# Performance work log

Hardware: AMD Instinct MI355X
Metric: run time of the kernel (lower is better)

The kernel has to match this reference:

```python
import jax, jax.numpy as jnp
import numpy as np

B, T, D, HD = 256, 256, 512, 64  # batch, seq_len(SEQ_LEN), EMBED_DIM, head_dim


def setup_inputs() -> dict:
    key = jax.random.key(0)
    k1, k2, k3, k4 = jax.random.split(key, 4)
    scale = D ** -0.5  # roughly matches nn.Linear init variance
    return {
        "x": jax.random.normal(k1, (B, T, D), dtype=jnp.float32),
        "Wq": jax.random.normal(k2, (HD, D), dtype=jnp.float32) * scale,
        "Wk": jax.random.normal(k3, (HD, D), dtype=jnp.float32) * scale,
        "Wv": jax.random.normal(k4, (HD, D), dtype=jnp.float32) * scale,
    }


def reference(x, Wq, Wk, Wv):
    # q,k,v: [B, T, HD]  (torch Linear: x @ W.T, no bias)
    q = jnp.einsum("btd,hd->bth", x, Wq)
    k = jnp.einsum("btd,hd->bth", x, Wk)
    v = jnp.einsum("btd,hd->bth", x, Wv)
    head_dim = Wq.shape[0]
    # scores: [B, T, T], scaled by head_dim^-0.5
    scores = jnp.einsum("bqh,bkh->bqk", q, k) * (head_dim ** -0.5)
    T_ = x.shape[1]
    causal = jnp.tril(jnp.ones((T_, T_), dtype=bool))  # tril[:T,:T] == 0 -> -inf
    scores = jnp.where(causal, scores, -jnp.inf)
    attn = jax.nn.softmax(scores, axis=-1)
    # dropout is identity in eval mode (reference baseline)
    return jnp.einsum("bqk,bkh->bqh", attn, v)
```

## Files before the change

kernel.cpp:

```cpp
#include <hip/hip_runtime.h>
#include <hip/hip_bf16.h>
#include <stdint.h>

#define NB 256
#define NT 256
#define ND 512
#define NH 64

typedef __bf16 bf16;
typedef __bf16 bf16x4 __attribute__((ext_vector_type(4)));
typedef __bf16 bf16x8 __attribute__((ext_vector_type(8)));
typedef float f32x4 __attribute__((ext_vector_type(4)));

static __device__ __forceinline__ f32x4 mfma16(bf16x8 a, bf16x8 b, f32x4 c) {
    return __builtin_amdgcn_mfma_f32_16x16x32_bf16(a, b, c, 0, 0, 0);
}

static __device__ __forceinline__ bf16x8 cvt8(f32x4 a, f32x4 b) {
    bf16x8 r;
    r[0] = (bf16)a.x; r[1] = (bf16)a.y; r[2] = (bf16)a.z; r[3] = (bf16)a.w;
    r[4] = (bf16)b.x; r[5] = (bf16)b.y; r[6] = (bf16)b.z; r[7] = (bf16)b.w;
    return r;
}

__global__ __launch_bounds__(256) void wconv_kernel(
        const float* __restrict__ Wq, const float* __restrict__ Wk,
        const float* __restrict__ Wv, bf16* __restrict__ wbf) {
    int idx = (blockIdx.x * 256 + threadIdx.x) * 4;
    const float* src;
    if (idx < 64 * ND)       src = Wq + idx;
    else if (idx < 128 * ND) src = Wk + (idx - 64 * ND);
    else                     src = Wv + (idx - 128 * ND);
    f32x4 v = *reinterpret_cast<const f32x4*>(src);
    bf16x4 o;
    o[0] = (bf16)v.x; o[1] = (bf16)v.y; o[2] = (bf16)v.z; o[3] = (bf16)v.w;
    *reinterpret_cast<bf16x4*>(wbf + idx) = o;
}

__global__ __launch_bounds__(256) void qkv_gemm_kernel(
        const float* __restrict__ x, const bf16* __restrict__ wbf,
        bf16* __restrict__ qws, bf16* __restrict__ kws, bf16* __restrict__ vt) {
    __shared__ alignas(16) char lds[65536];
    const int t = threadIdx.x;
    const int lane = t & 63, wave = t >> 6;
    const long m0 = (long)blockIdx.x * 64;

    {
        const int srow = t >> 2, skc = (t & 3) * 16;
        const int ssw = (srow & 7) << 4;
        const float* xsrc = x + (m0 + srow) * ND + skc;
        #pragma unroll
        for (int kk = 0; kk < ND; kk += 64) {
            f32x4 a = *reinterpret_cast<const f32x4*>(xsrc + kk);
            f32x4 b = *reinterpret_cast<const f32x4*>(xsrc + kk + 4);
            f32x4 c = *reinterpret_cast<const f32x4*>(xsrc + kk + 8);
            f32x4 d = *reinterpret_cast<const f32x4*>(xsrc + kk + 12);
            int base = srow * 1024 + (kk + skc) * 2;
            *reinterpret_cast<bf16x8*>(lds + (base ^ ssw)) = cvt8(a, b);
            *reinterpret_cast<bf16x8*>(lds + ((base + 16) ^ ssw)) = cvt8(c, d);
        }
    }
    __syncthreads();

    f32x4 acc[4][3] = {};
    const int l15 = lane & 15, g8 = (lane >> 4) * 8;

    #pragma unroll 4
    for (int chunk = 0; chunk < 16; ++chunk) {
        const int kg = chunk * 32 + g8;
        bf16x8 Af[4];
        #pragma unroll
        for (int ri = 0; ri < 4; ++ri) {
            int row = ri * 16 + l15;
            Af[ri] = *reinterpret_cast<const bf16x8*>(
                lds + ((row * 1024 + kg * 2) ^ ((row & 7) << 4)));
        }
        #pragma unroll
        for (int ci = 0; ci < 3; ++ci) {
            int n = wave * 48 + ci * 16 + l15;
            bf16x8 Bf = *reinterpret_cast<const bf16x8*>(wbf + n * ND + kg);
            #pragma unroll
            for (int ri = 0; ri < 4; ++ri)
                acc[ri][ci] = mfma16(Af[ri], Bf, acc[ri][ci]);
        }
    }

    const int b = blockIdx.x >> 2;
    const int tb = (blockIdx.x & 3) * 64;
    #pragma unroll
    for (int ci = 0; ci < 3; ++ci) {
        int n = wave * 48 + ci * 16 + l15;
        int sel = n >> 6, hd = n & 63;
        #pragma unroll
        for (int ri = 0; ri < 4; ++ri) {
            #pragma unroll
            for (int r = 0; r < 4; ++r) {
                int trow = tb + ri * 16 + (lane >> 4) * 4 + r;
                long grow = m0 + ri * 16 + (lane >> 4) * 4 + r;
                float val = acc[ri][ci][r];
                if (sel == 0)      qws[grow * NH + hd] = (bf16)(val * 0.125f);
                else if (sel == 1) kws[grow * NH + hd] = (bf16)val;
                else               vt[((long)b * NH + hd) * NT + trow] = (bf16)val;
            }
        }
    }
}

__global__ __launch_bounds__(64) void attn_kernel(
        const bf16* __restrict__ qws, const bf16* __restrict__ kws,
        const bf16* __restrict__ vt, float* __restrict__ out) {
    __shared__ alignas(16) char plds[8192];
    const int lane = threadIdx.x & 63;
    const int l15 = lane & 15, g = lane >> 4;
    const int qt = blockIdx.x, b = blockIdx.y;
    const long bbase = (long)b * NT;

    const int nct = qt + 1;
    const int nch = (nct + 1) >> 1;

    bf16x8 Qf[2];
    {
        long qrow = bbase + qt * 16 + l15;
        const bf16* qsrc = qws + qrow * NH + g * 8;
        Qf[0] = *reinterpret_cast<const bf16x8*>(qsrc);
        Qf[1] = *reinterpret_cast<const bf16x8*>(qsrc + 32);
    }

    const int qrow0 = qt * 16 + g * 4;
    float sum[4] = {0.f, 0.f, 0.f, 0.f};
    f32x4 O[4] = {};

    #pragma unroll
    for (int ch = 0; ch < 8; ++ch) {
        if (ch < nch) {
            const int t0 = 2 * ch, t1 = 2 * ch + 1;
            const bool t1v = (t1 < nct);
            f32x4 S0 = {}, S1 = {};
            {
                const bf16* kb0 = kws + (bbase + t0 * 16 + l15) * NH + g * 8;
                S0 = mfma16(Qf[0], *reinterpret_cast<const bf16x8*>(kb0), S0);
                S0 = mfma16(Qf[1], *reinterpret_cast<const bf16x8*>(kb0 + 32), S0);
                if (t1v) {
                    const bf16* kb1 = kb0 + 16 * NH;
                    S1 = mfma16(Qf[0], *reinterpret_cast<const bf16x8*>(kb1), S1);
                    S1 = mfma16(Qf[1], *reinterpret_cast<const bf16x8*>(kb1 + 32), S1);
                }
            }
            const int c0 = t0 * 16 + l15, c1 = c0 + 16;
            #pragma unroll
            for (int r = 0; r < 4; ++r) {
                int rowp = g * 4 + r;
                int sw = (rowp & 7) << 4;
                float p0 = (c0 <= qrow0 + r) ? __expf(S0[r]) : 0.0f;
                sum[r] += p0;
                *reinterpret_cast<bf16*>(plds + ((rowp * 512 + c0 * 2) ^ sw)) = (bf16)p0;
                float p1 = (t1v && c1 <= qrow0 + r) ? __expf(S1[r]) : 0.0f;
                sum[r] += p1;
                *reinterpret_cast<bf16*>(plds + ((rowp * 512 + c1 * 2) ^ sw)) = (bf16)p1;
            }
            const int k0 = ch * 32 + g * 8;
            bf16x8 Pf = *reinterpret_cast<const bf16x8*>(
                plds + ((l15 * 512 + k0 * 2) ^ ((l15 & 7) << 4)));
            #pragma unroll
            for (int cb = 0; cb < 4; ++cb) {
                int hd = cb * 16 + l15;
                bf16x8 Vf = *reinterpret_cast<const bf16x8*>(
                    vt + ((long)b * NH + hd) * NT + k0);
                O[cb] = mfma16(Pf, Vf, O[cb]);
            }
        }
    }

    #pragma unroll
    for (int r = 0; r < 4; ++r) {
        sum[r] += __shfl_xor(sum[r], 1);
        sum[r] += __shfl_xor(sum[r], 2);
        sum[r] += __shfl_xor(sum[r], 4);
        sum[r] += __shfl_xor(sum[r], 8);
        sum[r] = 1.0f / sum[r];
    }

    #pragma unroll
    for (int cb = 0; cb < 4; ++cb) {
        int hd = cb * 16 + l15;
        #pragma unroll
        for (int r = 0; r < 4; ++r) {
            long orow = bbase + qt * 16 + g * 4 + r;
            out[orow * NH + hd] = O[cb][r] * sum[r];
        }
    }
}

extern "C" void kernel_launch(void* const* d_in, const int* in_sizes, int n_in,
                              void* d_out, int out_size, void* d_ws, size_t ws_size,
                              hipStream_t stream) {
    const float* x  = (const float*)d_in[0];
    const float* Wq = (const float*)d_in[1];
    const float* Wk = (const float*)d_in[2];
    const float* Wv = (const float*)d_in[3];
    float* out = (float*)d_out;

    char* ws = (char*)d_ws;
    bf16* wbf = (bf16*)ws;
    bf16* qws = (bf16*)(ws + 0x30000);
    bf16* kws = (bf16*)(ws + 0x30000 + 8388608);
    bf16* vt  = (bf16*)(ws + 0x30000 + 2 * 8388608);

    wconv_kernel<<<96, 256, 0, stream>>>(Wq, Wk, Wv, wbf);
    qkv_gemm_kernel<<<1024, 256, 0, stream>>>(x, wbf, qws, kws, vt);
    attn_kernel<<<dim3(16, NB), 64, 0, stream>>>(qws, kws, vt, out);
}
```

Before: 259.1 us.

## Double-buffer x via direct global-to-LDS loads; batch attention per sequence with LDS-staged K

The QKV GEMM now streams x in fp32 straight into LDS with global_load_lds, double-buffered in 64-column stages, and converts to bf16 at fragment-read time. This overlaps the next stage's loads with the current stage's MFMAs and halves LDS use so more blocks fit per CU. The attention kernel now runs one 256-thread block per batch element, stages that sequence's K once into swizzled LDS, and gives each wave a balanced set of causal query tiles (wave, 7-wave, 8+wave, 15-wave). The trade is fewer, larger blocks (256 instead of 4096) and extra LDS traffic for fp32 x, in exchange for reusing K and spreading causal work evenly across waves.

```diff
diff --git a/kernel.cpp b/kernel.cpp
--- a/kernel.cpp
+++ b/kernel.cpp
@@ -21,6 +21,12 @@
     r[0] = (bf16)a.x; r[1] = (bf16)a.y; r[2] = (bf16)a.z; r[3] = (bf16)a.w;
     r[4] = (bf16)b.x; r[5] = (bf16)b.y; r[6] = (bf16)b.z; r[7] = (bf16)b.w;
     return r;
+}
+
+static __device__ __forceinline__ void gload_lds16(const void* g, void* l) {
+    __builtin_amdgcn_global_load_lds(
+        (const __attribute__((address_space(1))) void*)g,
+        (__attribute__((address_space(3))) void*)l, 16, 0, 0);
 }
 
 __global__ __launch_bounds__(256) void wconv_kernel(
@@ -37,52 +43,63 @@
     *reinterpret_cast<bf16x4*>(wbf + idx) = o;
 }
 
-__global__ __launch_bounds__(256) void qkv_gemm_kernel(
+__global__ __launch_bounds__(256, 4) void qkv_gemm_kernel(
         const float* __restrict__ x, const bf16* __restrict__ wbf,
         bf16* __restrict__ qws, bf16* __restrict__ kws, bf16* __restrict__ vt) {
-    __shared__ alignas(16) char lds[65536];
-    const int t = threadIdx.x;
-    const int lane = t & 63, wave = t >> 6;
+    __shared__ alignas(16) char lds[32768];
+    const int t = threadIdx.x, lane = t & 63, wave = t >> 6;
+    const int l15 = lane & 15, g = lane >> 4;
     const long m0 = (long)blockIdx.x * 64;
-
-    {
-        const int srow = t >> 2, skc = (t & 3) * 16;
-        const int ssw = (srow & 7) << 4;
-        const float* xsrc = x + (m0 + srow) * ND + skc;
-        #pragma unroll
-        for (int kk = 0; kk < ND; kk += 64) {
-            f32x4 a = *reinterpret_cast<const f32x4*>(xsrc + kk);
-            f32x4 b = *reinterpret_cast<const f32x4*>(xsrc + kk + 4);
-            f32x4 c = *reinterpret_cast<const f32x4*>(xsrc + kk + 8);
-            f32x4 d = *reinterpret_cast<const f32x4*>(xsrc + kk + 12);
-            int base = srow * 1024 + (kk + skc) * 2;
-            *reinterpret_cast<bf16x8*>(lds + (base ^ ssw)) = cvt8(a, b);
-            *reinterpret_cast<bf16x8*>(lds + ((base + 16) ^ ssw)) = cvt8(c, d);
-        }
-    }
+    const char* xb = (const char*)x;
+
+    f32x4 acc[4][3] = {};
+
+    #pragma unroll
+    for (int i = 0; i < 4; ++i) {
+        int row = wave * 16 + i * 4 + g;
+        const char* src = xb + (m0 + row) * 2048 + ((l15 * 16) ^ ((row & 7) << 4));
+        gload_lds16(src, lds + (wave * 4 + i) * 1024);
+    }
+    asm volatile("s_waitcnt vmcnt(0)");
     __syncthreads();
 
-    f32x4 acc[4][3] = {};
-    const int l15 = lane & 15, g8 = (lane >> 4) * 8;
-
-    #pragma unroll 4
-    for (int chunk = 0; chunk < 16; ++chunk) {
-        const int kg = chunk * 32 + g8;
-        bf16x8 Af[4];
-        #pragma unroll
-        for (int ri = 0; ri < 4; ++ri) {
-            int row = ri * 16 + l15;
-            Af[ri] = *reinterpret_cast<const bf16x8*>(
-                lds + ((row * 1024 + kg * 2) ^ ((row & 7) << 4)));
-        }
-        #pragma unroll
-        for (int ci = 0; ci < 3; ++ci) {
-            int n = wave * 48 + ci * 16 + l15;
-            bf16x8 Bf = *reinterpret_cast<const bf16x8*>(wbf + n * ND + kg);
-            #pragma unroll
-            for (int ri = 0; ri < 4; ++ri)
-                acc[ri][ci] = mfma16(Af[ri], Bf, acc[ri][ci]);
-        }
+    #pragma unroll
+    for (int s = 0; s < 8; ++s) {
+        const int cbuf = (s & 1) * 16384;
+        if (s < 7) {
+            const int nbuf = ((s + 1) & 1) * 16384;
+            #pragma unroll
+            for (int i = 0; i < 4; ++i) {
+                int row = wave * 16 + i * 4 + g;
+                const char* src = xb + (m0 + row) * 2048 + (long)(s + 1) * 256
+                                + ((l15 * 16) ^ ((row & 7) << 4));
+                gload_lds16(src, lds + nbuf + (wave * 4 + i) * 1024);
+            }
+        }
+        #pragma unroll
+        for (int k2 = 0; k2 < 2; ++k2) {
+            const int cbyte = (k2 * 32 + g * 8) * 4;
+            bf16x8 Af[4];
+            #pragma unroll
+            for (int ri = 0; ri < 4; ++ri) {
+                int row = ri * 16 + l15;
+                int sw = (row & 7) << 4;
+                f32x4 lo = *reinterpret_cast<const f32x4*>(lds + cbuf + row * 256 + (cbyte ^ sw));
+                f32x4 hi = *reinterpret_cast<const f32x4*>(lds + cbuf + row * 256 + ((cbyte + 16) ^ sw));
+                Af[ri] = cvt8(lo, hi);
+            }
+            const int kg = s * 64 + k2 * 32 + g * 8;
+            #pragma unroll
+            for (int ci = 0; ci < 3; ++ci) {
+                int n = wave * 48 + ci * 16 + l15;
+                bf16x8 Bf = *reinterpret_cast<const bf16x8*>(wbf + n * ND + kg);
+                #pragma unroll
+                for (int ri = 0; ri < 4; ++ri)
+                    acc[ri][ci] = mfma16(Af[ri], Bf, acc[ri][ci]);
+            }
+        }
+        asm volatile("s_waitcnt vmcnt(0)");
+        __syncthreads();
     }
 
     const int b = blockIdx.x >> 2;
@@ -95,8 +112,8 @@
         for (int ri = 0; ri < 4; ++ri) {
             #pragma unroll
             for (int r = 0; r < 4; ++r) {
-                int trow = tb + ri * 16 + (lane >> 4) * 4 + r;
-                long grow = m0 + ri * 16 + (lane >> 4) * 4 + r;
+                int trow = tb + ri * 16 + g * 4 + r;
+                long grow = m0 + ri * 16 + g * 4 + r;
                 float val = acc[ri][ci][r];
                 if (sel == 0)      qws[grow * NH + hd] = (bf16)(val * 0.125f);
                 else if (sel == 1) kws[grow * NH + hd] = (bf16)val;
@@ -106,87 +123,100 @@
     }
 }
 
-__global__ __launch_bounds__(64) void attn_kernel(
+__global__ __launch_bounds__(256) void attn_kernel(
         const bf16* __restrict__ qws, const bf16* __restrict__ kws,
         const bf16* __restrict__ vt, float* __restrict__ out) {
-    __shared__ alignas(16) char plds[8192];
-    const int lane = threadIdx.x & 63;
+    __shared__ alignas(16) char lds[65536];
+    const int t = threadIdx.x, lane = t & 63, wave = t >> 6;
     const int l15 = lane & 15, g = lane >> 4;
-    const int qt = blockIdx.x, b = blockIdx.y;
+    const int b = blockIdx.x;
     const long bbase = (long)b * NT;
 
-    const int nct = qt + 1;
-    const int nch = (nct + 1) >> 1;
-
-    bf16x8 Qf[2];
     {
-        long qrow = bbase + qt * 16 + l15;
-        const bf16* qsrc = qws + qrow * NH + g * 8;
-        Qf[0] = *reinterpret_cast<const bf16x8*>(qsrc);
-        Qf[1] = *reinterpret_cast<const bf16x8*>(qsrc + 32);
-    }
-
-    const int qrow0 = qt * 16 + g * 4;
-    float sum[4] = {0.f, 0.f, 0.f, 0.f};
-    f32x4 O[4] = {};
-
-    #pragma unroll
-    for (int ch = 0; ch < 8; ++ch) {
-        if (ch < nch) {
-            const int t0 = 2 * ch, t1 = 2 * ch + 1;
-            const bool t1v = (t1 < nct);
+        const bf16* src = kws + (bbase + t) * NH;
+        char* dstrow = lds + t * 128;
+        int sw = (t & 7) << 4;
+        #pragma unroll
+        for (int j = 0; j < 8; ++j) {
+            bf16x8 v = *reinterpret_cast<const bf16x8*>(src + j * 8);
+            *reinterpret_cast<bf16x8*>(dstrow + ((j * 16) ^ sw)) = v;
+        }
+    }
+    __syncthreads();
+
+    char* plds = lds + 32768 + wave * 8192;
+    const int qts[4] = {wave, 7 - wave, 8 + wave, 15 - wave};
+
+    #pragma unroll
+    for (int qi = 0; qi < 4; ++qi) {
+        const int qt = qts[qi];
+        const int nct = qt + 1, nch = (nct + 1) >> 1;
+        bf16x8 Qf0, Qf1;
+        {
+            const bf16* qsrc = qws + (bbase + qt * 16 + l15) * NH + g * 8;
+            Qf0 = *reinterpret_cast<const bf16x8*>(qsrc);
+            Qf1 = *reinterpret_cast<const bf16x8*>(qsrc + 32);
+        }
+        const int qrow0 = qt * 16 + g * 4;
+        float sum[4] = {0.f, 0.f, 0.f, 0.f};
+        f32x4 O[4] = {};
+
+        for (int ch = 0; ch < nch; ++ch) {
+            const int c0 = ch * 32 + l15;
+            const int c1 = c0 + 16;
+            const bool t1v = (2 * ch + 1) < nct;
             f32x4 S0 = {}, S1 = {};
             {
-                const bf16* kb0 = kws + (bbase + t0 * 16 + l15) * NH + g * 8;
-                S0 = mfma16(Qf[0], *reinterpret_cast<const bf16x8*>(kb0), S0);
-                S0 = mfma16(Qf[1], *reinterpret_cast<const bf16x8*>(kb0 + 32), S0);
+                const char* k0p = lds + c0 * 128;
+                int sw0 = (c0 & 7) << 4;
+                S0 = mfma16(Qf0, *reinterpret_cast<const bf16x8*>(k0p + ((g * 16) ^ sw0)), S0);
+                S0 = mfma16(Qf1, *reinterpret_cast<const bf16x8*>(k0p + ((64 + g * 16) ^ sw0)), S0);
                 if (t1v) {
-                    const bf16* kb1 = kb0 + 16 * NH;
-                    S1 = mfma16(Qf[0], *reinterpret_cast<const bf16x8*>(kb1), S1);
-                    S1 = mfma16(Qf[1], *reinterpret_cast<const bf16x8*>(kb1 + 32), S1);
+                    const char* k1p = lds + c1 * 128;
+                    int sw1 = (c1 & 7) << 4;
+                    S1 = mfma16(Qf0, *reinterpret_cast<const bf16x8*>(k1p + ((g * 16) ^ sw1)), S1);
+                    S1 = mfma16(Qf1, *reinterpret_cast<const bf16x8*>(k1p + ((64 + g * 16) ^ sw1)), S1);
                 }
             }
-            const int c0 = t0 * 16 + l15, c1 = c0 + 16;
             #pragma unroll
             for (int r = 0; r < 4; ++r) {
                 int rowp = g * 4 + r;
-                int sw = (rowp & 7) << 4;
+                int swp = (rowp & 7) << 4;
                 float p0 = (c0 <= qrow0 + r) ? __expf(S0[r]) : 0.0f;
                 sum[r] += p0;
-                *reinterpret_cast<bf16*>(plds + ((rowp * 512 + c0 * 2) ^ sw)) = (bf16)p0;
+                *reinterpret_cast<bf16*>(plds + ((rowp * 512 + c0 * 2) ^ swp)) = (bf16)p0;
                 float p1 = (t1v && c1 <= qrow0 + r) ? __expf(S1[r]) : 0.0f;
                 sum[r] += p1;
-                *reinterpret_cast<bf16*>(plds + ((rowp * 512 + c1 * 2) ^ sw)) = (bf16)p1;
+                *reinterpret_cast<bf16*>(plds + ((rowp * 512 + c1 * 2) ^ swp)) = (bf16)p1;
             }
             const int k0 = ch * 32 + g * 8;
             bf16x8 Pf = *reinterpret_cast<const bf16x8*>(
                 plds + ((l15 * 512 + k0 * 2) ^ ((l15 & 7) << 4)));
             #pragma unroll
-            for (int cb = 0; cb < 4; ++cb) {
-                int hd = cb * 16 + l15;
+            for (int cb2 = 0; cb2 < 4; ++cb2) {
+                int hd = cb2 * 16 + l15;
                 bf16x8 Vf = *reinterpret_cast<const bf16x8*>(
                     vt + ((long)b * NH + hd) * NT + k0);
-                O[cb] = mfma16(Pf, Vf, O[cb]);
-            }
-        }
-    }
-
-    #pragma unroll
-    for (int r = 0; r < 4; ++r) {
-        sum[r] += __shfl_xor(sum[r], 1);
-        sum[r] += __shfl_xor(sum[r], 2);
-        sum[r] += __shfl_xor(sum[r], 4);
-        sum[r] += __shfl_xor(sum[r], 8);
-        sum[r] = 1.0f / sum[r];
-    }
-
-    #pragma unroll
-    for (int cb = 0; cb < 4; ++cb) {
-        int hd = cb * 16 + l15;
+                O[cb2] = mfma16(Pf, Vf, O[cb2]);
+            }
+        }
+
         #pragma unroll
         for (int r = 0; r < 4; ++r) {
-            long orow = bbase + qt * 16 + g * 4 + r;
-            out[orow * NH + hd] = O[cb][r] * sum[r];
+            sum[r] += __shfl_xor(sum[r], 1);
+            sum[r] += __shfl_xor(sum[r], 2);
+            sum[r] += __shfl_xor(sum[r], 4);
+            sum[r] += __shfl_xor(sum[r], 8);
+            sum[r] = 1.0f / sum[r];
+        }
+        #pragma unroll
+        for (int cb2 = 0; cb2 < 4; ++cb2) {
+            int hd = cb2 * 16 + l15;
+            #pragma unroll
+            for (int r = 0; r < 4; ++r) {
+                long orow = bbase + qt * 16 + g * 4 + r;
+                out[orow * NH + hd] = O[cb2][r] * sum[r];
+            }
         }
     }
 }
@@ -208,5 +238,5 @@
 
     wconv_kernel<<<96, 256, 0, stream>>>(Wq, Wk, Wv, wbf);
     qkv_gemm_kernel<<<1024, 256, 0, stream>>>(x, wbf, qws, kws, vt);
-    attn_kernel<<<dim3(16, NB), 64, 0, stream>>>(qws, kws, vt, out);
-}
+    attn_kernel<<<NB, 256, 0, stream>>>(qws, kws, vt, out);
+}
```

Measured after the change: 231.6 us. 10.6% less time.
